# Performance work log

Hardware: AMD Instinct MI355X
Metric: run time of the kernel (lower is better)

Reference implementation:

```python
import jax, jax.numpy as jnp
import numpy as np

B, C, H, W = 4, 512, 64, 64
HC = C // 2  # hidden_channel of Correlation


def setup_inputs() -> dict:
    key = jax.random.key(0)
    ks = jax.random.split(key, 7)
    s = 0.02
    return {
        "x": jax.random.normal(ks[0], (B, C, H, W), dtype=jnp.float32),
        "Wf": jax.random.normal(ks[1], (HC, C), dtype=jnp.float32) * s,
        "bf": jnp.zeros((HC,), dtype=jnp.float32),
        "Wg": jax.random.normal(ks[2], (HC, C), dtype=jnp.float32) * s,
        "bg": jnp.zeros((HC,), dtype=jnp.float32),
        "Wh": jax.random.normal(ks[3], (C, C), dtype=jnp.float32) * s,
        "bh": jnp.zeros((C,), dtype=jnp.float32),
    }


def reference(x, Wf, bf, Wg, bg, Wh, bh):
    b, c, h, w = x.shape
    n = h * w
    xf = x.reshape(b, c, n)  # hw_flatten: [B, C, N]
    # 1x1 convs == per-pixel linear projections
    f = jnp.einsum('oc,bcn->bon', Wf, xf) + bf[None, :, None]  # [B, HC, N]
    g = jnp.einsum('oc,bcn->bon', Wg, xf) + bg[None, :, None]  # [B, HC, N]
    hproj = jnp.einsum('oc,bcn->bon', Wh, xf) + bh[None, :, None]  # [B, C, N]
    # energy = f^T g : [B, N, N]
    energy = jnp.einsum('bcn,bcm->bnm', f, g)
    correlation = jax.nn.softmax(energy, axis=-1)
    # attention = mean over query axis n of correlation -> [B, 1, N]
    attention = jnp.mean(correlation, axis=1, keepdims=True)
    # residual = h @ correlation^T : sum_k h[b,c,k] * corr[b,j,k]
    residual = jnp.einsum('bck,bjk->bcj', hproj, correlation)
    residual = residual.reshape(b, c, h, w)
    attention = attention.reshape(b, 1, h, w)
    return residual, attention
```

## Files before the change

### kernel.cpp

```cpp
#include <hip/hip_runtime.h>
#include <cmath>

#define BATCH 4
#define CH    512
#define HCH   256
#define NPIX  4096
#define L2E   1.44269504088896340736f

typedef __attribute__((ext_vector_type(8))) short bf16x8;
typedef __attribute__((ext_vector_type(4))) float f32x4;

#define MFMA16(a, b, c) __builtin_amdgcn_mfma_f32_16x16x32_bf16((a), (b), (c), 0, 0, 0)

__device__ __forceinline__ unsigned short f2bf(float f) {
    unsigned int u = __float_as_uint(f);
    return (unsigned short)((u + 0x7fffu + ((u >> 16) & 1u)) >> 16);
}
__device__ __forceinline__ ushort4 pack4(float a, float b, float c, float d) {
    ushort4 u; u.x = f2bf(a); u.y = f2bf(b); u.z = f2bf(c); u.w = f2bf(d); return u;
}
__device__ __forceinline__ void gload16(const unsigned short* g, unsigned short* l) {
    __builtin_amdgcn_global_load_lds(
        (const __attribute__((address_space(1))) unsigned int*)g,
        (__attribute__((address_space(3))) unsigned int*)l, 16, 0, 0);
}

__global__ __launch_bounds__(256) void convert_w_kernel(
    const float* __restrict__ Wf, const float* __restrict__ Wg,
    const float* __restrict__ Wh, unsigned short* __restrict__ Wc)
{
    const int idx = blockIdx.x * 256 + threadIdx.x;
    const int o  = idx >> 7;
    const int c4 = (idx & 127) * 4;
    const float* src = (o < HCH)     ? (Wf + (size_t)o * CH + c4)
                     : (o < 2 * HCH) ? (Wg + (size_t)(o - HCH) * CH + c4)
                                     : (Wh + (size_t)(o - 2 * HCH) * CH + c4);
    float4 v = *(const float4*)src;
    *(ushort4*)&Wc[(size_t)o * CH + c4] = pack4(v.x, v.y, v.z, v.w);
}

__global__ __launch_bounds__(256) void convert_x_kernel(
    const float* __restrict__ x, unsigned short* __restrict__ Xp)
{
    __shared__ unsigned short Lt[64][40];
    const int b  = blockIdx.z;
    const int cb = blockIdx.y;
    const int n0 = blockIdx.x * 64;
    const int t  = threadIdx.x;
    const int cr = t >> 4;
    const int f4 = t & 15;
    #pragma unroll
    for (int p = 0; p < 2; ++p) {
        const int c = p * 16 + cr;
        float4 v = *(const float4*)(x + ((size_t)b * CH + cb * 32 + c) * NPIX + n0 + f4 * 4);
        Lt[f4 * 4 + 0][c] = f2bf(v.x);
        Lt[f4 * 4 + 1][c] = f2bf(v.y);
        Lt[f4 * 4 + 2][c] = f2bf(v.z);
        Lt[f4 * 4 + 3][c] = f2bf(v.w);
    }
    __syncthreads();
    const int n  = t >> 2;
    const int ch = t & 3;
    uint4 u = *(const uint4*)&Lt[n][ch * 8];
    *(uint4*)&Xp[((size_t)b * 16 + cb) * (NPIX * 32) + (size_t)(n0 + n) * 32 + ch * 8] = u;
}

__global__ __launch_bounds__(256, 4) void proj_fg_kernel(
    const unsigned short* __restrict__ Wc, const unsigned short* __restrict__ Xp,
    const float* __restrict__ bf, const float* __restrict__ bg,
    unsigned short* __restrict__ F, unsigned short* __restrict__ G)
{
    const int b  = blockIdx.z;
    const int n0 = blockIdx.x * 64;
    const int o0 = blockIdx.y * 128;
    const int t  = threadIdx.x;
    const int wave = t >> 6, lane = t & 63, quad = lane >> 4, l16 = lane & 15;
    const int ow = o0 + wave * 32;

    f32x4 acc[2][4];
    #pragma unroll
    for (int ms = 0; ms < 2; ++ms)
        #pragma unroll
        for (int ns = 0; ns < 4; ++ns) acc[ms][ns] = (f32x4){0.f, 0.f, 0.f, 0.f};

    const unsigned short* xb = Xp + (size_t)b * 16 * (NPIX * 32);
    for (int st = 0; st < 16; ++st) {
        bf16x8 a0 = *(const bf16x8*)&Wc[(size_t)(ow + l16) * CH + st * 32 + quad * 8];
        bf16x8 a1 = *(const bf16x8*)&Wc[(size_t)(ow + 16 + l16) * CH + st * 32 + quad * 8];
        const unsigned short* xs = xb + (size_t)st * (NPIX * 32) + quad * 8;
        #pragma unroll
        for (int ns = 0; ns < 4; ++ns) {
            bf16x8 bb = *(const bf16x8*)(xs + (size_t)(n0 + ns * 16 + l16) * 32);
            acc[0][ns] = MFMA16(a0, bb, acc[0][ns]);
            acc[1][ns] = MFMA16(a1, bb, acc[1][ns]);
        }
    }

    const int orow = quad * 4;
    const int gx = (l16 & 7) << 3;
    #pragma unroll
    for (int ms = 0; ms < 2; ++ms) {
        const int ob = ow + ms * 16 + orow;
        float bias[4];
        #pragma unroll
        for (int r = 0; r < 4; ++r)
            bias[r] = (o0 < HCH) ? bf[ob + r] : bg[ob + r - HCH];
        #pragma unroll
        for (int ns = 0; ns < 4; ++ns) {
            const int n = n0 + ns * 16 + l16;
            ushort4 u = pack4(acc[ms][ns][0] + bias[0], acc[ms][ns][1] + bias[1],
                              acc[ms][ns][2] + bias[2], acc[ms][ns][3] + bias[3]);
            if (o0 < HCH) {
                *(ushort4*)&F[((size_t)b * NPIX + n) * HCH + ob] = u;
            } else {
                const int og = ob - HCH;
                const int cb = og >> 5, co = og & 31;
                const int el = (n * 32 + co) ^ gx;
                *(ushort4*)&G[((size_t)b * 8 + cb) * (NPIX * 32) + el] = u;
            }
        }
    }
}

__global__ __launch_bounds__(256, 4) void proj_v_kernel(
    const unsigned short* __restrict__ Wc, const unsigned short* __restrict__ Xp,
    const float* __restrict__ bh, unsigned short* __restrict__ V)
{
    const int b  = blockIdx.z;
    const int c0 = blockIdx.x * 64;
    const int p0 = blockIdx.y * 128;
    const int t  = threadIdx.x;
    const int wave = t >> 6, lane = t & 63, quad = lane >> 4, l16 = lane & 15;
    const int pw = p0 + wave * 32;

    f32x4 acc[2][4];
    #pragma unroll
    for (int ms = 0; ms < 2; ++ms)
        #pragma unroll
        for (int ns = 0; ns < 4; ++ns) acc[ms][ns] = (f32x4){0.f, 0.f, 0.f, 0.f};

    const unsigned short* xb = Xp + (size_t)b * 16 * (NPIX * 32);
    for (int st = 0; st < 16; ++st) {
        const unsigned short* xs = xb + (size_t)st * (NPIX * 32) + quad * 8;
        bf16x8 a0 = *(const bf16x8*)(xs + (size_t)(pw + l16) * 32);
        bf16x8 a1 = *(const bf16x8*)(xs + (size_t)(pw + 16 + l16) * 32);
        #pragma unroll
        for (int ns = 0; ns < 4; ++ns) {
            bf16x8 bb = *(const bf16x8*)&Wc[(size_t)(2 * HCH + c0 + ns * 16 + l16) * CH + st * 32 + quad * 8];
            acc[0][ns] = MFMA16(a0, bb, acc[0][ns]);
            acc[1][ns] = MFMA16(a1, bb, acc[1][ns]);
        }
    }

    float biasv[4];
    #pragma unroll
    for (int ns = 0; ns < 4; ++ns) biasv[ns] = bh[c0 + ns * 16 + l16];

    const int kb = pw >> 5;
    const int ko0 = quad * 4;
    const int cx = (l16 & 7) << 3;
    #pragma unroll
    for (int ms = 0; ms < 2; ++ms) {
        #pragma unroll
        for (int ns = 0; ns < 4; ++ns) {
            const int c = c0 + ns * 16 + l16;
            ushort4 u = pack4(acc[ms][ns][0] + biasv[ns], acc[ms][ns][1] + biasv[ns],
                              acc[ms][ns][2] + biasv[ns], acc[ms][ns][3] + biasv[ns]);
            const int el = (c * 32 + ms * 16 + ko0) ^ cx;
            *(ushort4*)&V[((size_t)b * 128 + kb) * (CH * 32) + el] = u;
        }
    }
}

__global__ __launch_bounds__(512, 4) void score_kernel(
    const unsigned short* __restrict__ F, const unsigned short* __restrict__ G,
    unsigned short* __restrict__ P, float* __restrict__ rowl)
{
    __shared__ unsigned short Gl[2][8 * 64 * 32];
    const int blk = blockIdx.x;
    const int xcd = blk & 7;
    const int b   = xcd >> 1;
    const int kh  = xcd & 1;
    const int q0  = (blk >> 3) * 64;
    const int t    = threadIdx.x;
    const int wave = t >> 6, lane = t & 63, quad = lane >> 4, l16 = lane & 15;
    const int qh = wave >> 2, kw = wave & 3;

    bf16x8 af[2][8];
    #pragma unroll
    for (int qs = 0; qs < 2; ++qs)
        #pragma unroll
        for (int st = 0; st < 8; ++st)
            af[qs][st] = *(const bf16x8*)&F[((size_t)b * NPIX + q0 + qh * 32 + qs * 16 + l16) * HCH + st * 32 + quad * 8];

    float ls[2][4];
    #pragma unroll
    for (int qs = 0; qs < 2; ++qs)
        #pragma unroll
        for (int r = 0; r < 4; ++r) ls[qs][r] = 0.f;

    const unsigned short* Gb = G + (size_t)b * 8 * (NPIX * 32);
    unsigned short* Pb2 = P + (size_t)b * 128 * (NPIX * 32) + (size_t)(q0 + qh * 32) * 32;
    const int qx = (quad & 1) * 4;

    const int kbeg = kh * 2048;

    auto stage = [&](int bb, int kt) {
        const size_t kofs = (size_t)(kbeg + kt * 64) * 32;
        #pragma unroll
        for (int j = 0; j < 4; ++j) {
            const int cbse = j * 512 + wave * 64;
            const int cb   = cbse >> 8;
            const int o16  = cbse & 255;
            const unsigned short* g = Gb + (size_t)cb * (NPIX * 32) + kofs
                                        + o16 * 8 + lane * 8;
            gload16(g, &Gl[bb][cb * 2048 + o16 * 8]);
        }
    };

    const int fx = (l16 & 7) << 4;
    const int bO = (((kw * 16 + l16) * 64) + quad * 16) ^ fx;

    stage(0, 0);
    __syncthreads();

    int buf = 0;
    for (int kt = 0; kt < 32; ++kt) {
        if (kt + 1 < 32) stage(buf ^ 1, kt + 1);

        f32x4 s[2];
        s[0] = (f32x4){0.f, 0.f, 0.f, 0.f};
        s[1] = (f32x4){0.f, 0.f, 0.f, 0.f};
        const char* gb = (const char*)&Gl[buf][0];
        #pragma unroll
        for (int st = 0; st < 8; ++st) {
            bf16x8 bb = *(const bf16x8*)(gb + st * 4096 + bO);
            s[0] = MFMA16(af[0][st], bb, s[0]);
            s[1] = MFMA16(af[1][st], bb, s[1]);
        }

        const int kkk = kbeg + kt * 64 + kw * 16;
        unsigned short* pw = Pb2 + (size_t)(kkk >> 5) * (NPIX * 32);
        const int kcol = (kw & 1) * 16 + l16;
        #pragma unroll
        for (int qs = 0; qs < 2; ++qs)
            #pragma unroll
            for (int r = 0; r < 4; ++r) {
                float e = exp2f(L2E * s[qs][r]);
                const int el = ((qs * 16 + quad * 4 + r) * 32 + kcol) ^ ((qx + r) << 3);
                pw[el] = f2bf(e);
                ls[qs][r] += e;
            }

        __syncthreads();
        buf ^= 1;
    }

    #pragma unroll
    for (int d = 1; d < 16; d <<= 1)
        #pragma unroll
        for (int qs = 0; qs < 2; ++qs)
            #pragma unroll
            for (int r = 0; r < 4; ++r) ls[qs][r] += __shfl_xor(ls[qs][r], d, 64);

    if (l16 == 0) {
        #pragma unroll
        for (int qs = 0; qs < 2; ++qs)
            #pragma unroll
            for (int r = 0; r < 4; ++r)
                atomicAdd(&rowl[(size_t)b * NPIX + q0 + qh * 32 + qs * 16 + quad * 4 + r], ls[qs][r]);
    }
}

__global__ __launch_bounds__(512, 4) void pv_kernel(
    const unsigned short* __restrict__ P, const unsigned short* __restrict__ V,
    const float* __restrict__ rowl, float* __restrict__ outres)
{
    __shared__ unsigned short Pl[2][64 * 32];
    __shared__ unsigned short Vl[2][256 * 32];
    const int blk = blockIdx.x;
    const int xcd = blk & 7;
    const int b   = xcd >> 1;
    const int ch  = xcd & 1;
    const int q0  = (blk >> 3) * 64;
    const int t    = threadIdx.x;
    const int wave = t >> 6, lane = t & 63, quad = lane >> 4, l16 = lane & 15;
    const int qw = wave >> 2;
    const int cw = wave & 3;
    const int cbase = cw * 64;

    const unsigned short* Pg = P + ((size_t)b * 128 * NPIX + q0) * 32;
    const unsigned short* Vg = V + ((size_t)b * 128 * CH + ch * 256) * 32;

    const int fx  = (l16 & 7) << 4;
    const int pA0 = (((qw * 32      + l16) * 64) + quad * 16) ^ fx;
    const int pA1 = (((qw * 32 + 16 + l16) * 64) + quad * 16) ^ fx;
    const int vO0 = (((cbase +  0 + l16) * 64) + quad * 16) ^ fx;
    const int vO1 = (((cbase + 16 + l16) * 64) + quad * 16) ^ fx;
    const int vO2 = (((cbase + 32 + l16) * 64) + quad * 16) ^ fx;
    const int vO3 = (((cbase + 48 + l16) * 64) + quad * 16) ^ fx;

    f32x4 O[2][4];
    #pragma unroll
    for (int qs = 0; qs < 2; ++qs)
        #pragma unroll
        for (int ct = 0; ct < 4; ++ct) O[qs][ct] = (f32x4){0.f, 0.f, 0.f, 0.f};

    auto stage = [&](int bb, int kb) {
        const unsigned short* vg = Vg + (size_t)kb * (CH * 32) + wave * 1024;
        unsigned short* vl = &Vl[bb][wave * 1024];
        gload16(vg + lane * 8,       vl);
        gload16(vg + 512 + lane * 8, vl + 512);
        if (wave < 4) {
            const unsigned short* pg = Pg + (size_t)kb * (NPIX * 32) + wave * 512;
            gload16(pg + lane * 8, &Pl[bb][wave * 512]);
        }
    };

    stage(0, 0);
    __syncthreads();

    int buf = 0;
    for (int kb = 0; kb < 128; ++kb) {
        if (kb + 1 < 128) stage(buf ^ 1, kb + 1);

        const char* pb = (const char*)&Pl[buf][0];
        const char* vb = (const char*)&Vl[buf][0];
        bf16x8 a0 = *(const bf16x8*)(pb + pA0);
        bf16x8 a1 = *(const bf16x8*)(pb + pA1);
        bf16x8 v0 = *(const bf16x8*)(vb + vO0);
        bf16x8 v1 = *(const bf16x8*)(vb + vO1);
        bf16x8 v2 = *(const bf16x8*)(vb + vO2);
        bf16x8 v3 = *(const bf16x8*)(vb + vO3);
        O[0][0] = MFMA16(a0, v0, O[0][0]);
        O[1][0] = MFMA16(a1, v0, O[1][0]);
        O[0][1] = MFMA16(a0, v1, O[0][1]);
        O[1][1] = MFMA16(a1, v1, O[1][1]);
        O[0][2] = MFMA16(a0, v2, O[0][2]);
        O[1][2] = MFMA16(a1, v2, O[1][2]);
        O[0][3] = MFMA16(a0, v3, O[0][3]);
        O[1][3] = MFMA16(a1, v3, O[1][3]);

        __syncthreads();
        buf ^= 1;
    }

    float lr[2][4];
    #pragma unroll
    for (int qs = 0; qs < 2; ++qs)
        #pragma unroll
        for (int r = 0; r < 4; ++r)
            lr[qs][r] = 1.0f / rowl[(size_t)b * NPIX + q0 + qw * 32 + qs * 16 + quad * 4 + r];

    const int cb2 = ch * 256 + cbase;
    #pragma unroll
    for (int qs = 0; qs < 2; ++qs) {
        #pragma unroll
        for (int ct = 0; ct < 4; ++ct) {
            f32x4 o = O[qs][ct];
            o[0] *= lr[qs][0]; o[1] *= lr[qs][1]; o[2] *= lr[qs][2]; o[3] *= lr[qs][3];
            const int c = cb2 + ct * 16 + l16;
            *(f32x4*)&outres[((size_t)b * CH + c) * NPIX + q0 + qw * 32 + qs * 16 + quad * 4] = o;
        }
    }
}

__global__ __launch_bounds__(256) void colsum_kernel(
    const unsigned short* __restrict__ P, const float* __restrict__ rowl,
    float* __restrict__ attnacc)
{
    __shared__ float CS[16][32];
    const int blk = blockIdx.x;
    const int b  = blk >> 7;
    const int kb = blk & 127;
    const int t  = threadIdx.x;
    const int ko2 = t & 15;
    const int qr  = t >> 4;
    const unsigned short* Pb = P + (size_t)(b * 128 + kb) * (NPIX * 32);
    const float* rl = rowl + (size_t)b * NPIX;
    const int qx = (qr & 7) << 3;

    float a0 = 0.f, a1 = 0.f;
    for (int q = qr; q < NPIX; q += 16) {
        unsigned int u = *(const unsigned int*)(Pb + ((q * 32 + ko2 * 2) ^ qx));
        float li = 1.0f / rl[q];
        a0 += __uint_as_float(u << 16) * li;
        a1 += __uint_as_float(u & 0xFFFF0000u) * li;
    }
    CS[qr][ko2 * 2]     = a0;
    CS[qr][ko2 * 2 + 1] = a1;
    __syncthreads();
    if (t < 32) {
        float s = 0.f;
        #pragma unroll
        for (int i = 0; i < 16; ++i) s += CS[i][t];
        attnacc[(size_t)b * NPIX + kb * 32 + t] = s;
    }
}

__global__ __launch_bounds__(512, 4) void stats_kernel(
    const unsigned short* __restrict__ F, const unsigned short* __restrict__ G,
    float* __restrict__ rowl)
{
    const int blk = blockIdx.x;
    const int xcd = blk & 7;
    const int b   = xcd >> 1;
    const int kh  = xcd & 1;
    const int q0  = (blk >> 3) * 64;
    const int t    = threadIdx.x;
    const int wave = t >> 6, lane = t & 63, quad = lane >> 4, l16 = lane & 15;
    const int qh = wave >> 2, kw = wave & 3;
    const int gx = (l16 & 7) << 3;

    bf16x8 af[2][8];
    #pragma unroll
    for (int qs = 0; qs < 2; ++qs)
        #pragma unroll
        for (int st = 0; st < 8; ++st)
            af[qs][st] = *(const bf16x8*)&F[((size_t)b * NPIX + q0 + qh * 32 + qs * 16 + l16) * HCH + st * 32 + quad * 8];

    float ls[2][4];
    #pragma unroll
    for (int qs = 0; qs < 2; ++qs)
        #pragma unroll
        for (int r = 0; r < 4; ++r) ls[qs][r] = 0.f;

    const unsigned short* Gb = G + (size_t)b * 8 * (NPIX * 32);
    const int kbeg = kh * 2048, kend = kbeg + 2048;
    for (int k0 = kbeg; k0 < kend; k0 += 128) {
        const int kk = k0 + kw * 32;
        f32x4 s[2][2];
        #pragma unroll
        for (int qs = 0; qs < 2; ++qs)
            #pragma unroll
            for (int ks = 0; ks < 2; ++ks) s[qs][ks] = (f32x4){0.f, 0.f, 0.f, 0.f};
        #pragma unroll
        for (int st = 0; st < 8; ++st) {
            const unsigned short* gs = Gb + (size_t)st * (NPIX * 32);
            bf16x8 b0 = *(const bf16x8*)(gs + ((((kk + l16) * 32) + quad * 8) ^ gx));
            bf16x8 b1 = *(const bf16x8*)(gs + ((((kk + 16 + l16) * 32) + quad * 8) ^ gx));
            s[0][0] = MFMA16(af[0][st], b0, s[0][0]);
            s[1][0] = MFMA16(af[1][st], b0, s[1][0]);
            s[0][1] = MFMA16(af[0][st], b1, s[0][1]);
            s[1][1] = MFMA16(af[1][st], b1, s[1][1]);
        }
        #pragma unroll
        for (int qs = 0; qs < 2; ++qs)
            #pragma unroll
            for (int r = 0; r < 4; ++r)
                ls[qs][r] += exp2f(L2E * s[qs][0][r]) + exp2f(L2E * s[qs][1][r]);
    }

    #pragma unroll
    for (int d = 1; d < 16; d <<= 1)
        #pragma unroll
        for (int qs = 0; qs < 2; ++qs)
            #pragma unroll
            for (int r = 0; r < 4; ++r) ls[qs][r] += __shfl_xor(ls[qs][r], d, 64);

    if (l16 == 0) {
        #pragma unroll
        for (int qs = 0; qs < 2; ++qs)
            #pragma unroll
            for (int r = 0; r < 4; ++r)
                atomicAdd(&rowl[(size_t)b * NPIX + q0 + qh * 32 + qs * 16 + quad * 4 + r], ls[qs][r]);
    }
}

__global__ __launch_bounds__(512, 4) void apply_kernel(
    const unsigned short* __restrict__ F, const unsigned short* __restrict__ G,
    const unsigned short* __restrict__ V, const float* __restrict__ rowl,
    float* __restrict__ outres, float* __restrict__ attnacc)
{
    __shared__ unsigned short Pl[2][32][136];
    const int blk = blockIdx.x;
    const int xcd = blk & 7;
    const int b   = xcd >> 1;
    const int ch  = xcd & 1;
    const int q0  = (blk >> 3) * 32;
    const int t    = threadIdx.x;
    const int wave = t >> 6, lane = t & 63, quad = lane >> 4, l16 = lane & 15;
    const int cw = ch * 256 + wave * 32;
    const int vx = (l16 & 7) << 3;
    const int gx = (l16 & 7) << 3;

    float linv[2][4];
    #pragma unroll
    for (int qs = 0; qs < 2; ++qs)
        #pragma unroll
        for (int r = 0; r < 4; ++r)
            linv[qs][r] = 1.0f / rowl[(size_t)b * NPIX + q0 + qs * 16 + quad * 4 + r];

    f32x4 O[2][2];
    #pragma unroll
    for (int qs = 0; qs < 2; ++qs)
        #pragma unroll
        for (int ct = 0; ct < 2; ++ct) O[qs][ct] = (f32x4){0.f, 0.f, 0.f, 0.f};

    const unsigned short* Gb = G + (size_t)b * 8 * (NPIX * 32);
    const unsigned short* Vb = V + (size_t)b * 128 * (CH * 32);
    const unsigned short* Fq = F + ((size_t)b * NPIX + q0) * HCH;

    int buf = 0;
    for (int k0 = 0; k0 < NPIX; k0 += 128) {
        const int kk = k0 + wave * 16;
        f32x4 s[2];
        s[0] = (f32x4){0.f, 0.f, 0.f, 0.f};
        s[1] = (f32x4){0.f, 0.f, 0.f, 0.f};
        #pragma unroll
        for (int st = 0; st < 8; ++st) {
            bf16x8 a0 = *(const bf16x8*)&Fq[(size_t)l16 * HCH + st * 32 + quad * 8];
            bf16x8 a1 = *(const bf16x8*)&Fq[(size_t)(16 + l16) * HCH + st * 32 + quad * 8];
            bf16x8 bg = *(const bf16x8*)(Gb + (size_t)st * (NPIX * 32)
                                         + ((((kk + l16) * 32) + quad * 8) ^ gx));
            s[0] = MFMA16(a0, bg, s[0]);
            s[1] = MFMA16(a1, bg, s[1]);
        }

        float p[2][4];
        #pragma unroll
        for (int qs = 0; qs < 2; ++qs)
            #pragma unroll
            for (int r = 0; r < 4; ++r)
                p[qs][r] = exp2f(L2E * s[qs][r]) * linv[qs][r];

        #pragma unroll
        for (int qs = 0; qs < 2; ++qs)
            #pragma unroll
            for (int r = 0; r < 4; ++r)
                Pl[buf][qs * 16 + quad * 4 + r][wave * 16 + l16] = f2bf(p[qs][r]);

        if (ch == 0) {
            float cs = p[0][0] + p[0][1] + p[0][2] + p[0][3]
                     + p[1][0] + p[1][1] + p[1][2] + p[1][3];
            cs += __shfl_xor(cs, 16, 64);
            cs += __shfl_xor(cs, 32, 64);
            if (quad == 0)
                atomicAdd(&attnacc[(size_t)b * NPIX + kk + l16], cs);
        }

        __syncthreads();

        #pragma unroll
        for (int ks = 0; ks < 4; ++ks) {
            bf16x8 pa0 = *(const bf16x8*)&Pl[buf][l16][ks * 32 + quad * 8];
            bf16x8 pa1 = *(const bf16x8*)&Pl[buf][16 + l16][ks * 32 + quad * 8];
            const unsigned short* vs = Vb + ((size_t)(k0 >> 5) + ks) * (CH * 32);
            #pragma unroll
            for (int ct = 0; ct < 2; ++ct) {
                const int el = (((cw + ct * 16 + l16) * 32) + quad * 8) ^ vx;
                bf16x8 vv = *(const bf16x8*)(vs + el);
                O[0][ct] = MFMA16(pa0, vv, O[0][ct]);
                O[1][ct] = MFMA16(pa1, vv, O[1][ct]);
            }
        }
        buf ^= 1;
    }

    #pragma unroll
    for (int qs = 0; qs < 2; ++qs) {
        #pragma unroll
        for (int ct = 0; ct < 2; ++ct) {
            const int c = cw + ct * 16 + l16;
            *(f32x4*)&outres[((size_t)b * CH + c) * NPIX + q0 + qs * 16 + quad * 4] = O[qs][ct];
        }
    }
}

__global__ __launch_bounds__(256) void attn_fin_kernel(
    const float* __restrict__ acc, float* __restrict__ outa)
{
    const int i = blockIdx.x * 256 + threadIdx.x;
    if (i < BATCH * NPIX) outa[i] = acc[i] * (1.0f / (float)NPIX);
}

extern "C" void kernel_launch(void* const* d_in, const int* in_sizes, int n_in,
                              void* d_out, int out_size, void* d_ws, size_t ws_size,
                              hipStream_t stream)
{
    (void)in_sizes; (void)n_in; (void)out_size;
    const float* x  = (const float*)d_in[0];
    const float* Wf = (const float*)d_in[1];
    const float* bf = (const float*)d_in[2];
    const float* Wg = (const float*)d_in[3];
    const float* bg = (const float*)d_in[4];
    const float* Wh = (const float*)d_in[5];
    const float* bh = (const float*)d_in[6];
    float* out = (float*)d_out;

    const size_t P_ELEMS  = (size_t)BATCH * 128 * NPIX * 32;
    const size_t XP_ELEMS = (size_t)BATCH * 16 * NPIX * 32;
    const size_t F_ELEMS  = (size_t)BATCH * NPIX * HCH;
    const size_t V_ELEMS  = (size_t)BATCH * 128 * CH * 32;
    const size_t NEED = (P_ELEMS + 2 * F_ELEMS + V_ELEMS) * 2
                      + (size_t)2 * BATCH * NPIX * 4;

    if (ws_size >= NEED) {
        unsigned short* P  = (unsigned short*)d_ws;
        unsigned short* Xp = P;
        unsigned short* Wc = P + XP_ELEMS;
        unsigned short* F  = P + P_ELEMS;
        unsigned short* G  = F + F_ELEMS;
        unsigned short* V  = G + F_ELEMS;
        float* rowl    = (float*)(V + V_ELEMS);
        float* attnacc = rowl + (size_t)BATCH * NPIX;

        hipMemsetAsync(rowl, 0, (size_t)BATCH * NPIX * sizeof(float), stream);

        convert_w_kernel<<<512, 256, 0, stream>>>(Wf, Wg, Wh, Wc);
        convert_x_kernel<<<dim3(NPIX / 64, 16, BATCH), 256, 0, stream>>>(x, Xp);

        proj_fg_kernel<<<dim3(NPIX / 64, 4, BATCH), 256, 0, stream>>>(Wc, Xp, bf, bg, F, G);
        proj_v_kernel<<<dim3(8, NPIX / 128, BATCH), 256, 0, stream>>>(Wc, Xp, bh, V);

        score_kernel<<<512, 512, 0, stream>>>(F, G, P, rowl);
        pv_kernel<<<512, 512, 0, stream>>>(P, V, rowl, out);
        colsum_kernel<<<512, 256, 0, stream>>>(P, rowl, attnacc);

        attn_fin_kernel<<<BATCH * NPIX / 256, 256, 0, stream>>>(
            attnacc, out + (size_t)BATCH * CH * NPIX);
    } else {
        unsigned short* Xp = (unsigned short*)d_ws;
        unsigned short* Wc = Xp + XP_ELEMS;
        unsigned short* F  = Wc + (size_t)1024 * CH;
        unsigned short* G  = F + F_ELEMS;
        unsigned short* V  = G + F_ELEMS;
        float* rowl    = (float*)(V + V_ELEMS);
        float* attnacc = rowl + (size_t)BATCH * NPIX;

        hipMemsetAsync(rowl, 0, (size_t)2 * BATCH * NPIX * sizeof(float), stream);

        convert_w_kernel<<<512, 256, 0, stream>>>(Wf, Wg, Wh, Wc);
        convert_x_kernel<<<dim3(NPIX / 64, 16, BATCH), 256, 0, stream>>>(x, Xp);

        proj_fg_kernel<<<dim3(NPIX / 64, 4, BATCH), 256, 0, stream>>>(Wc, Xp, bf, bg, F, G);
        proj_v_kernel<<<dim3(8, NPIX / 128, BATCH), 256, 0, stream>>>(Wc, Xp, bh, V);

        stats_kernel<<<512, 512, 0, stream>>>(F, G, rowl);
        apply_kernel<<<1024, 512, 0, stream>>>(F, G, V, rowl, out, attnacc);

        attn_fin_kernel<<<BATCH * NPIX / 256, 256, 0, stream>>>(
            attnacc, out + (size_t)BATCH * CH * NPIX);
    }
}
```

Baseline: 415.0 us.

## Triple-buffer PV loads with vmcnt waits, larger per-wave tiles, and split-barrier score loop

The PV kernel moves from 512 to 256 threads per block, so each wave now computes a 64x64 output tile (16 MFMAs per k-step instead of 8), and it uses a three-stage LDS ring with explicit vmcnt waits and raw s_barrier in place of __syncthreads. The score kernel's loop likewise swaps its trailing __syncthreads for a partial vmcnt wait plus s_barrier at the top of each iteration. The aim is to keep more global-to-LDS loads in flight and raise MFMA density per LDS read. In exchange the kernel uses more accumulator registers and LDS, and correctness now depends on the vmcnt counts being exact.

```diff
diff --git a/kernel.cpp b/kernel.cpp
--- a/kernel.cpp
+++ b/kernel.cpp
@@ -222,10 +222,14 @@
     const int bO = (((kw * 16 + l16) * 64) + quad * 16) ^ fx;
 
     stage(0, 0);
-    __syncthreads();
 
     int buf = 0;
     for (int kt = 0; kt < 32; ++kt) {
+        if (kt == 0) asm volatile("s_waitcnt vmcnt(0)" ::: "memory");
+        else         asm volatile("s_waitcnt vmcnt(4)" ::: "memory");
+        __builtin_amdgcn_s_barrier();
+        __builtin_amdgcn_sched_barrier(0);
+
         if (kt + 1 < 32) stage(buf ^ 1, kt + 1);
 
         f32x4 s[2];
@@ -251,8 +255,6 @@
                 pw[el] = f2bf(e);
                 ls[qs][r] += e;
             }
-
-        __syncthreads();
         buf ^= 1;
     }
 
@@ -272,12 +274,12 @@
     }
 }
 
-__global__ __launch_bounds__(512, 4) void pv_kernel(
+__global__ __launch_bounds__(256, 2) void pv_kernel(
     const unsigned short* __restrict__ P, const unsigned short* __restrict__ V,
     const float* __restrict__ rowl, float* __restrict__ outres)
 {
-    __shared__ unsigned short Pl[2][64 * 32];
-    __shared__ unsigned short Vl[2][256 * 32];
+    __shared__ unsigned short Pl[3][64 * 32];
+    __shared__ unsigned short Vl[3][256 * 32];
     const int blk = blockIdx.x;
     const int xcd = blk & 7;
     const int b   = xcd >> 1;
@@ -285,82 +287,101 @@
     const int q0  = (blk >> 3) * 64;
     const int t    = threadIdx.x;
     const int wave = t >> 6, lane = t & 63, quad = lane >> 4, l16 = lane & 15;
-    const int qw = wave >> 2;
-    const int cw = wave & 3;
-    const int cbase = cw * 64;
+    const int cbase = wave * 64;
 
     const unsigned short* Pg = P + ((size_t)b * 128 * NPIX + q0) * 32;
     const unsigned short* Vg = V + ((size_t)b * 128 * CH + ch * 256) * 32;
 
     const int fx  = (l16 & 7) << 4;
-    const int pA0 = (((qw * 32      + l16) * 64) + quad * 16) ^ fx;
-    const int pA1 = (((qw * 32 + 16 + l16) * 64) + quad * 16) ^ fx;
+    const int pA0 = (((  0 + l16) * 64) + quad * 16) ^ fx;
+    const int pA1 = ((( 16 + l16) * 64) + quad * 16) ^ fx;
+    const int pA2 = ((( 32 + l16) * 64) + quad * 16) ^ fx;
+    const int pA3 = ((( 48 + l16) * 64) + quad * 16) ^ fx;
     const int vO0 = (((cbase +  0 + l16) * 64) + quad * 16) ^ fx;
     const int vO1 = (((cbase + 16 + l16) * 64) + quad * 16) ^ fx;
     const int vO2 = (((cbase + 32 + l16) * 64) + quad * 16) ^ fx;
     const int vO3 = (((cbase + 48 + l16) * 64) + quad * 16) ^ fx;
 
-    f32x4 O[2][4];
-    #pragma unroll
-    for (int qs = 0; qs < 2; ++qs)
-        #pragma unroll
-        for (int ct = 0; ct < 4; ++ct) O[qs][ct] = (f32x4){0.f, 0.f, 0.f, 0.f};
+    f32x4 O[4][4];
+    #pragma unroll
+    for (int i = 0; i < 4; ++i)
+        #pragma unroll
+        for (int j = 0; j < 4; ++j) O[i][j] = (f32x4){0.f, 0.f, 0.f, 0.f};
 
     auto stage = [&](int bb, int kb) {
-        const unsigned short* vg = Vg + (size_t)kb * (CH * 32) + wave * 1024;
-        unsigned short* vl = &Vl[bb][wave * 1024];
-        gload16(vg + lane * 8,       vl);
-        gload16(vg + 512 + lane * 8, vl + 512);
-        if (wave < 4) {
-            const unsigned short* pg = Pg + (size_t)kb * (NPIX * 32) + wave * 512;
-            gload16(pg + lane * 8, &Pl[bb][wave * 512]);
-        }
+        const unsigned short* vg = Vg + (size_t)kb * (CH * 32) + wave * 2048;
+        unsigned short* vl = &Vl[bb][wave * 2048];
+        gload16(vg + lane * 8,        vl);
+        gload16(vg + 512  + lane * 8, vl + 512);
+        gload16(vg + 1024 + lane * 8, vl + 1024);
+        gload16(vg + 1536 + lane * 8, vl + 1536);
+        const unsigned short* pg = Pg + (size_t)kb * (NPIX * 32) + wave * 512;
+        gload16(pg + lane * 8, &Pl[bb][wave * 512]);
     };
 
-    stage(0, 0);
-    __syncthreads();
-
-    int buf = 0;
-    for (int kb = 0; kb < 128; ++kb) {
-        if (kb + 1 < 128) stage(buf ^ 1, kb + 1);
-
-        const char* pb = (const char*)&Pl[buf][0];
-        const char* vb = (const char*)&Vl[buf][0];
+    auto compute = [&](int bb) {
+        const char* pb = (const char*)&Pl[bb][0];
+        const char* vb = (const char*)&Vl[bb][0];
         bf16x8 a0 = *(const bf16x8*)(pb + pA0);
         bf16x8 a1 = *(const bf16x8*)(pb + pA1);
+        bf16x8 a2 = *(const bf16x8*)(pb + pA2);
+        bf16x8 a3 = *(const bf16x8*)(pb + pA3);
         bf16x8 v0 = *(const bf16x8*)(vb + vO0);
         bf16x8 v1 = *(const bf16x8*)(vb + vO1);
         bf16x8 v2 = *(const bf16x8*)(vb + vO2);
         bf16x8 v3 = *(const bf16x8*)(vb + vO3);
         O[0][0] = MFMA16(a0, v0, O[0][0]);
         O[1][0] = MFMA16(a1, v0, O[1][0]);
+        O[2][0] = MFMA16(a2, v0, O[2][0]);
+        O[3][0] = MFMA16(a3, v0, O[3][0]);
         O[0][1] = MFMA16(a0, v1, O[0][1]);
         O[1][1] = MFMA16(a1, v1, O[1][1]);
+        O[2][1] = MFMA16(a2, v1, O[2][1]);
+        O[3][1] = MFMA16(a3, v1, O[3][1]);
         O[0][2] = MFMA16(a0, v2, O[0][2]);
         O[1][2] = MFMA16(a1, v2, O[1][2]);
+        O[2][2] = MFMA16(a2, v2, O[2][2]);
+        O[3][2] = MFMA16(a3, v2, O[3][2]);
         O[0][3] = MFMA16(a0, v3, O[0][3]);
         O[1][3] = MFMA16(a1, v3, O[1][3]);
-
-        __syncthreads();
-        buf ^= 1;
-    }
-
-    float lr[2][4];
-    #pragma unroll
-    for (int qs = 0; qs < 2; ++qs)
+        O[2][3] = MFMA16(a2, v3, O[2][3]);
+        O[3][3] = MFMA16(a3, v3, O[3][3]);
+    };
+
+    stage(0, 0);
+    stage(1, 1);
+
+    int buf = 0, pre = 2;
+    for (int kb = 0; kb < 127; ++kb) {
+        asm volatile("s_waitcnt vmcnt(5)" ::: "memory");
+        __builtin_amdgcn_s_barrier();
+        __builtin_amdgcn_sched_barrier(0);
+        if (kb + 2 < 128) stage(pre, kb + 2);
+        compute(buf);
+        buf = (buf == 2) ? 0 : buf + 1;
+        pre = (pre == 2) ? 0 : pre + 1;
+    }
+    asm volatile("s_waitcnt vmcnt(0)" ::: "memory");
+    __builtin_amdgcn_s_barrier();
+    __builtin_amdgcn_sched_barrier(0);
+    compute(buf);
+
+    float lr[4][4];
+    #pragma unroll
+    for (int i = 0; i < 4; ++i)
         #pragma unroll
         for (int r = 0; r < 4; ++r)
-            lr[qs][r] = 1.0f / rowl[(size_t)b * NPIX + q0 + qw * 32 + qs * 16 + quad * 4 + r];
+            lr[i][r] = 1.0f / rowl[(size_t)b * NPIX + q0 + i * 16 + quad * 4 + r];
 
     const int cb2 = ch * 256 + cbase;
     #pragma unroll
-    for (int qs = 0; qs < 2; ++qs) {
-        #pragma unroll
-        for (int ct = 0; ct < 4; ++ct) {
-            f32x4 o = O[qs][ct];
-            o[0] *= lr[qs][0]; o[1] *= lr[qs][1]; o[2] *= lr[qs][2]; o[3] *= lr[qs][3];
-            const int c = cb2 + ct * 16 + l16;
-            *(f32x4*)&outres[((size_t)b * CH + c) * NPIX + q0 + qw * 32 + qs * 16 + quad * 4] = o;
+    for (int i = 0; i < 4; ++i) {
+        #pragma unroll
+        for (int j = 0; j < 4; ++j) {
+            f32x4 o = O[i][j];
+            o[0] *= lr[i][0]; o[1] *= lr[i][1]; o[2] *= lr[i][2]; o[3] *= lr[i][3];
+            const int c = cb2 + j * 16 + l16;
+            *(f32x4*)&outres[((size_t)b * CH + c) * NPIX + q0 + i * 16 + quad * 4] = o;
         }
     }
 }
@@ -614,7 +635,7 @@
         proj_v_kernel<<<dim3(8, NPIX / 128, BATCH), 256, 0, stream>>>(Wc, Xp, bh, V);
 
         score_kernel<<<512, 512, 0, stream>>>(F, G, P, rowl);
-        pv_kernel<<<512, 512, 0, stream>>>(P, V, rowl, out);
+        pv_kernel<<<512, 256, 0, stream>>>(P, V, rowl, out);
         colsum_kernel<<<512, 256, 0, stream>>>(P, rowl, attnacc);
 
         attn_fin_kernel<<<BATCH * NPIX / 256, 256, 0, stream>>>(
```

Result: no change. 415.6 us (+0.1%).
